# Kernel tuning notes

Measured on AMD Instinct MI355X. Metric: run time of the kernel, lower is better.

## Reference

```python
import jax, jax.numpy as jnp
import numpy as np

N, E, B, BLOCK = 100000, 1600000, 8, 12500
IN, HID, K, OUT = 128, 128, 4, 2
EPS = 1e-15


def setup_inputs() -> dict:
    key = jax.random.key(0)
    ks = jax.random.split(key, 14)
    x = jax.random.normal(ks[0], (N, IN), jnp.float32)
    # edges constrained within each graph's contiguous node block
    src = jax.random.randint(ks[1], (E,), 0, N)
    off = jax.random.randint(ks[2], (E,), 0, BLOCK)
    dst = (src // BLOCK) * BLOCK + off
    edge_index = jnp.stack([src, dst])
    batch = jnp.arange(N) // BLOCK
    s = 0.02
    params = dict(
        W_root1=jax.random.normal(ks[3], (IN, HID), jnp.float32) * s,
        W_rel1=jax.random.normal(ks[4], (IN, HID), jnp.float32) * s,
        b_rel1=jnp.zeros((HID,), jnp.float32),
        W_pool=jax.random.normal(ks[5], (HID, K), jnp.float32) * s,
        b_pool=jnp.zeros((K,), jnp.float32),
        W_rel3=jax.random.normal(ks[6], (HID, HID), jnp.float32) * s,
        b_rel3=jnp.zeros((HID,), jnp.float32),
        W_root3=jax.random.normal(ks[7], (HID, HID), jnp.float32) * s,
        W_lin1=jax.random.normal(ks[8], (HID, HID), jnp.float32) * s,
        b_lin1=jnp.zeros((HID,), jnp.float32),
        W_lin2=jax.random.normal(ks[9], (HID, OUT), jnp.float32) * s,
        b_lin2=jnp.zeros((OUT,), jnp.float32),
    )
    return dict(x=x, edge_index=edge_index, batch=batch, **params)


def _forward(x, edge_index, batch, W_root1, W_rel1, b_rel1, W_pool, b_pool,
             W_rel3, b_rel3, W_root3, W_lin1, b_lin1, W_lin2, b_lin2):
    src, dst = edge_index[0], edge_index[1]
    # GraphConv (aggr='add'): lin_rel(sum_j x_j) + lin_root(x)
    agg = jax.ops.segment_sum(x[src], dst, num_segments=N)  # [N, IN]
    h = jax.nn.relu(agg @ W_rel1 + b_rel1 + x @ W_root1)    # [N, HID]
    # cluster assignment
    s = jax.nn.softmax(h @ W_pool + b_pool, axis=-1)        # [N, K]
    # pooled node features: out[b] = S_b^T X_b  -> [B, K, HID]
    out = jax.ops.segment_sum(s[:, :, None] * h[:, None, :], batch, num_segments=B)
    # coarsened adjacency: out_adj[b] = S_b^T A_b S_b (A[dst, src] = 1 per edge)
    e_graph = batch[dst]
    contrib = s[dst][:, :, None] * s[src][:, None, :]       # [E, K, K]
    out_adj = jax.ops.segment_sum(contrib, e_graph, num_segments=B)  # [B, K, K]
    # mincut loss
    mincut_num = jnp.einsum('bkk->b', out_adj)
    deg = jax.ops.segment_sum(jnp.ones((E,), x.dtype), dst, num_segments=N)
    mincut_den = jax.ops.segment_sum(deg * jnp.sum(s * s, axis=-1), batch, num_segments=B)
    mc_loss = jnp.mean(-(mincut_num / mincut_den))
    # orthogonality loss
    ss = jax.ops.segment_sum(s[:, :, None] * s[:, None, :], batch, num_segments=B)  # [B,K,K]
    ss_norm = jnp.linalg.norm(ss, axis=(1, 2), keepdims=True)
    i_s = jnp.eye(K, dtype=x.dtype)
    o_loss = jnp.mean(jnp.linalg.norm(ss / ss_norm - i_s / jnp.sqrt(jnp.float32(K)), axis=(1, 2)))
    # fix and normalize coarsened adjacency
    out_adj = out_adj * (1.0 - i_s)  # zero diagonal
    d = jnp.sqrt(jnp.sum(out_adj, axis=-1)) + EPS  # [B, K]
    out_adj = out_adj / d[:, None, :] / d[:, :, None]
    # DenseGraphConv (aggr='add'): lin_rel(adj @ x) + lin_root(x)
    x2 = jnp.einsum('bkl,blc->bkc', out_adj, out) @ W_rel3 + b_rel3 + out @ W_root3
    x2 = jnp.mean(x2, axis=1)  # [B, HID]
    x2 = jax.nn.relu(x2 @ W_lin1 + b_lin1)
    logits = x2 @ W_lin2 + b_lin2
    return jax.nn.log_softmax(logits, axis=-1), mc_loss, o_loss, s, out_adj


def reference(x, edge_index, batch, W_root1, W_rel1, b_rel1, W_pool, b_pool,
              W_rel3, b_rel3, W_root3, W_lin1, b_lin1, W_lin2, b_lin2):
    return _forward(x, edge_index, batch, W_root1, W_rel1, b_rel1, W_pool, b_pool,
                    W_rel3, b_rel3, W_root3, W_lin1, b_lin1, W_lin2, b_lin2)
```

## Files before the change

kernel.cpp:

```cpp
#include <hip/hip_runtime.h>

#define NN     100000
#define EE     1600000
#define NB     8
#define BLK    12500
#define HID    128
#define KC     4
#define CHUNKS 196
#define NTILE  49
#define NBIN   392
#define GCAPS  5120

typedef __attribute__((ext_vector_type(8))) short bf16x8;
typedef __attribute__((ext_vector_type(4))) float f32x4;

__device__ __forceinline__ ushort f2bf(float f) {
  uint u = __float_as_uint(f);
  return (ushort)((u + 0x7FFFu + ((u >> 16) & 1u)) >> 16);
}
__device__ __forceinline__ float bf2f(ushort h) {
  return __uint_as_float(((uint)h) << 16);
}

#define GLL16(g, l) \
  __builtin_amdgcn_global_load_lds((const __attribute__((address_space(1))) void*)(g), \
                                   (__attribute__((address_space(3))) void*)(l), 16, 0, 0)

__global__ __launch_bounds__(256) void k_prep(const float4* __restrict__ x4,
                                              ushort* __restrict__ xb,
                                              const float* __restrict__ Wrel1,
                                              const float* __restrict__ Wroot1,
                                              ushort* __restrict__ Wt,
                                              uint* __restrict__ zbase) {
  const int bi = blockIdx.x;
  const int t = threadIdx.x;
  if (bi < 12500) {
    int i = bi * 256 + t;
    float4 v = x4[i];
    ushort4 r;
    r.x = f2bf(v.x); r.y = f2bf(v.y); r.z = f2bf(v.z); r.w = f2bf(v.w);
    *(ushort4*)(xb + (size_t)i * 4) = r;
  } else if (bi < 12628) {
    int col = bi - 12500, k = t;
    float v = (k < 128) ? Wrel1[k * 128 + col] : Wroot1[(k - 128) * 128 + col];
    Wt[col * 256 + k] = f2bf(v);
  } else {
    for (int i = t; i < 4912; i += 256) zbase[i] = 0u;
  }
}

__global__ __launch_bounds__(256) void k_bucket2(const int* __restrict__ ei,
                                                 int* __restrict__ sbcnt,
                                                 uint* __restrict__ gbuf) {
  __shared__ uint stage[8192];
  __shared__ int cnt[NBIN], start[NBIN + 1], rbase[NBIN];
  __shared__ int gtot[8], gb[8];
  const int t = threadIdx.x;
  for (int b = t; b < NBIN; b += 256) cnt[b] = 0;
  __syncthreads();
  const int e0 = blockIdx.x * 8192;
  uint pk[32]; int br[32];
#pragma unroll
  for (int i = 0; i < 32; ++i) {
    int e = e0 + i * 256 + t;
    bool val = (e < EE);
    int src = 0, dst = 0;
    if (val) {
      src = __builtin_nontemporal_load(ei + e);
      dst = __builtin_nontemporal_load(ei + EE + e);
    }
    int g = dst / BLK;
    int dl = dst - g * BLK;
    int sl = src - g * BLK;
    int bin = g * NTILE + (dl >> 8);
    pk[i] = ((uint)sl << 16) | (uint)dl;
    br[i] = val ? ((bin << 14) | atomicAdd(&cnt[bin], 1)) : -1;
  }
  __syncthreads();
  if (t < 8) {
    int s = 0;
    for (int k = 0; k < NTILE; ++k) s += cnt[t * NTILE + k];
    gtot[t] = s;
  }
  __syncthreads();
  if (t == 0) {
    int s = 0;
    for (int g = 0; g < 8; ++g) { gb[g] = s; s += gtot[g]; }
    start[NBIN] = s;
  }
  __syncthreads();
  if (t < 8) {
    int run = gb[t];
    for (int k = 0; k < NTILE; ++k) { start[t * NTILE + k] = run; run += cnt[t * NTILE + k]; }
  }
  __syncthreads();
  for (int b = t; b < NBIN; b += 256) rbase[b] = atomicAdd(&sbcnt[b], cnt[b]);
#pragma unroll
  for (int i = 0; i < 32; ++i) {
    if (br[i] >= 0) {
      int bin = br[i] >> 14, rank = br[i] & 16383;
      stage[start[bin] + rank] = pk[i];
    }
  }
  __syncthreads();
  for (int b = t; b < NBIN; b += 256) {
    const int n = cnt[b];
    const int s0 = start[b];
    uint* dst = gbuf + (size_t)b * GCAPS + rbase[b];
    for (int i = 0; i < n; ++i) dst[i] = stage[s0 + i];
  }
}

__global__ __launch_bounds__(256) void k_csr_tile(const uint* __restrict__ gbuf,
                                                  const int* __restrict__ sbcnt,
                                                  int* __restrict__ rowptr,
                                                  int* __restrict__ count,
                                                  int* __restrict__ csr) {
  const int g = blockIdx.x & 7;
  const int tile = blockIdx.x >> 3;
  const int bin = g * NTILE + tile;
  const int m = sbcnt[bin];
  const int n0t = tile * 256;
  const int nt = min(256, BLK - n0t);
  __shared__ uint ent[GCAPS];
  __shared__ ushort srt[GCAPS];
  __shared__ int cnt[256], scn[256], cur[256];
  __shared__ int red[256];
  const int t = threadIdx.x;
  {
    int partial = 0;
    for (int i = t; i < bin; i += 256) partial += sbcnt[i];
    red[t] = partial;
    __syncthreads();
    for (int off = 128; off > 0; off >>= 1) {
      if (t < off) red[t] += red[t + off];
      __syncthreads();
    }
  }
  const int base = red[0];
  cnt[t] = 0;
  __syncthreads();
  const uint* buf = gbuf + (size_t)bin * GCAPS;
  for (int i = t; i < m; i += 256) {
    uint pk = buf[i];
    ent[i] = pk;
    atomicAdd(&cnt[(int)(pk & 0xFFFFu) - n0t], 1);
  }
  __syncthreads();
  int v = cnt[t];
  scn[t] = v;
  __syncthreads();
  for (int s = 1; s < 256; s <<= 1) {
    int x = (t >= s) ? scn[t - s] : 0;
    __syncthreads();
    scn[t] += x;
    __syncthreads();
  }
  int excl = scn[t] - v;
  cur[t] = excl;
  if (t < nt) {
    rowptr[g * BLK + n0t + t] = base + excl;
    count[g * BLK + n0t + t] = v;
  }
  __syncthreads();
  for (int i = t; i < m; i += 256) {
    uint pk = ent[i];
    int p = atomicAdd(&cur[(int)(pk & 0xFFFFu) - n0t], 1);
    srt[p] = (ushort)(pk >> 16);
  }
  __syncthreads();
  const int nb = g * BLK;
  for (int i = t; i < m; i += 256)
    csr[base + i] = nb + (int)srt[i];
}

__global__ __launch_bounds__(256) void k_agg2(const ushort* __restrict__ xb,
                                              const int* __restrict__ count,
                                              const int* __restrict__ rowptr,
                                              const int* __restrict__ csr,
                                              const ushort* __restrict__ zrow,
                                              ushort* __restrict__ aggb) {
  const int xg = blockIdx.x & 7;
  const int j = blockIdx.x >> 3;
  const int half = threadIdx.x >> 5;
  const int lane = threadIdx.x & 31;
  const int ln = j * 8 + half;
  if (ln >= BLK) return;
  const int node = xg * BLK + ln;
  const int deg = count[node];
  const int* sl = csr + rowptr[node];
  int idx0 = (lane < deg) ? sl[lane] : 0;
  int idx1 = (32 + lane < deg) ? sl[32 + lane] : 0;
  const ushort* zr = zrow + lane * 4;

  float4 acc[8];
#pragma unroll
  for (int q = 0; q < 8; ++q) acc[q] = (float4){0.f, 0.f, 0.f, 0.f};

  const int nb8 = (deg + 7) >> 3;
  for (int b = 0; b < nb8; ++b) {
    const int e = b * 8;
    const ushort* ps[8];
#pragma unroll
    for (int q = 0; q < 8; ++q) {
      int ee = e + q;
      int si = (ee < 32) ? __shfl(idx0, ee, 32)
             : ((ee < 64) ? __shfl(idx1, ee - 32, 32)
                          : ((ee < deg) ? sl[ee] : 0));
      ps[q] = (ee < deg) ? (xb + (size_t)si * HID + lane * 4) : zr;
    }
    uint2 v[8];
#pragma unroll
    for (int q = 0; q < 8; ++q) v[q] = *(const uint2*)ps[q];
#pragma unroll
    for (int q = 0; q < 8; ++q) {
      acc[q].x += __uint_as_float(v[q].x << 16);
      acc[q].y += __uint_as_float(v[q].x & 0xFFFF0000u);
      acc[q].z += __uint_as_float(v[q].y << 16);
      acc[q].w += __uint_as_float(v[q].y & 0xFFFF0000u);
    }
  }

  float lo0 = 0.f, hi0 = 0.f, lo1 = 0.f, hi1 = 0.f;
#pragma unroll
  for (int q = 0; q < 8; ++q) { lo0 += acc[q].x; hi0 += acc[q].y; lo1 += acc[q].z; hi1 += acc[q].w; }
  ushort4 r;
  r.x = f2bf(lo0); r.y = f2bf(hi0); r.z = f2bf(lo1); r.w = f2bf(hi1);
  *(ushort4*)(aggb + (size_t)node * HID + lane * 4) = r;
}

__global__ __launch_bounds__(256) void k_gemm(
    const ushort* __restrict__ aggb, const ushort* __restrict__ xb,
    const ushort* __restrict__ Wt, const float* __restrict__ brel1,
    ushort* __restrict__ hbuf) {
  __shared__ ushort Aag_s[64][128];
  __shared__ ushort Ax_s[64][128];
  __shared__ ushort hLb[64][136];

  const int t = threadIdx.x;
  const int bi = blockIdx.x;
  const int bG = bi & 7;
  const int chunk = bi >> 3;
  const int node0 = bG * BLK + chunk * 64;
  int nrows = BLK - chunk * 64;
  if (nrows > 64) nrows = 64;

  const int w = t >> 6;
  const int l = t & 63;

  {
    const int sub = l >> 4;
    const int c16 = l & 15;
#pragma unroll
    for (int i = 0; i < 4; ++i) {
      const int j = w * 4 + i;
      const int row = j * 4 + sub;
      const int rs = (row < nrows) ? row : (nrows - 1);
      const int boff = (c16 * 16) ^ ((row & 7) << 4);
      const ushort* ga = aggb + (size_t)(node0 + rs) * HID + (boff >> 1);
      const ushort* gx = xb + (size_t)(node0 + rs) * HID + (boff >> 1);
      GLL16(ga, &Aag_s[j * 4][0]);
      GLL16(gx, &Ax_s[j * 4][0]);
    }
  }

  const int m16 = l & 15;
  const int gq = l >> 4;

  bf16x8 Breg[8][2];
#pragma unroll
  for (int kt = 0; kt < 8; ++kt)
#pragma unroll
    for (int fc = 0; fc < 2; ++fc)
      Breg[kt][fc] =
          *(const bf16x8*)(Wt + (size_t)(32 * w + 16 * fc + m16) * 256 + kt * 32 + 8 * gq);

  f32x4 acc[4][2];
#pragma unroll
  for (int fr = 0; fr < 4; ++fr)
#pragma unroll
    for (int fc = 0; fc < 2; ++fc) acc[fr][fc] = (f32x4){0.f, 0.f, 0.f, 0.f};

  asm volatile("s_waitcnt vmcnt(0)" ::: "memory");
  __syncthreads();

#pragma unroll
  for (int kt = 0; kt < 8; ++kt) {
    const int k4 = kt & 3;
    bf16x8 af[4];
#pragma unroll
    for (int fr = 0; fr < 4; ++fr) {
      const int r = 16 * fr + m16;
      const int ci = (k4 * 32 + gq * 8) ^ ((r & 7) << 3);
      af[fr] = (kt < 4) ? *(const bf16x8*)&Aag_s[r][ci]
                        : *(const bf16x8*)&Ax_s[r][ci];
    }
#pragma unroll
    for (int fr = 0; fr < 4; ++fr)
#pragma unroll
      for (int fc = 0; fc < 2; ++fc)
        acc[fr][fc] = __builtin_amdgcn_mfma_f32_16x16x32_bf16(af[fr], Breg[kt][fc],
                                                              acc[fr][fc], 0, 0, 0);
  }

  const float bc0 = brel1[32 * w + m16];
  const float bc1 = brel1[32 * w + 16 + m16];
#pragma unroll
  for (int fr = 0; fr < 4; ++fr)
#pragma unroll
    for (int fc = 0; fc < 2; ++fc)
#pragma unroll
      for (int r = 0; r < 4; ++r)
        hLb[16 * fr + 4 * gq + r][32 * w + 16 * fc + m16] =
            f2bf(fmaxf(acc[fr][fc][r] + (fc ? bc1 : bc0), 0.f));
  __syncthreads();

  {
    const int row = t >> 2;
    const int ch = (t & 3) * 32;
    if (row < nrows) {
      ushort* dst = hbuf + (size_t)(node0 + row) * HID + ch;
      const ushort* src = &hLb[row][ch];
#pragma unroll
      for (int q = 0; q < 4; ++q)
        *(bf16x8*)(dst + q * 8) = *(const bf16x8*)(src + q * 8);
    }
  }
}

__global__ __launch_bounds__(256) void k_epi(
    const ushort* __restrict__ hbuf, const float* __restrict__ Wpool,
    const float* __restrict__ bpool, const int* __restrict__ count,
    float* __restrict__ s_out, float* __restrict__ out_pool,
    float* __restrict__ ss_g, float* __restrict__ den_g) {
  __shared__ ushort hLb[64][136];
  __shared__ float outL[KC][HID];
  __shared__ float ssL[16];
  __shared__ float denL;

  const int t = threadIdx.x;
  const int bi = blockIdx.x;
  const int bG = bi & 7;
  const int chunk = bi >> 3;
  const int node0 = bG * BLK + chunk * 64;
  int nrows = BLK - chunk * 64;
  if (nrows > 64) nrows = 64;

  {
    const int row = t >> 2;
    const int ch = (t & 3) * 32;
    const int rs = (row < nrows) ? row : (nrows - 1);
    const ushort* src = hbuf + (size_t)(node0 + rs) * HID + ch;
    ushort* dst = &hLb[row][ch];
#pragma unroll
    for (int q = 0; q < 4; ++q)
      *(bf16x8*)(dst + q * 8) = *(const bf16x8*)(src + q * 8);
  }

  for (int i = t; i < KC * HID; i += 256) ((float*)outL)[i] = 0.f;
  if (t < 16) ssL[t] = 0.f;
  if (t == 0) denL = 0.f;
  __syncthreads();

  const int g4 = t >> 4;
  const int c0 = (t & 15) << 2;
  const int li = t & 15;

  float h[4][8];
#pragma unroll
  for (int r = 0; r < 4; ++r) {
    ushort4 v0 = *(const ushort4*)&hLb[g4 * 4 + r][c0];
    ushort4 v1 = *(const ushort4*)&hLb[g4 * 4 + r][c0 + 64];
    h[r][0] = bf2f(v0.x); h[r][1] = bf2f(v0.y); h[r][2] = bf2f(v0.z); h[r][3] = bf2f(v0.w);
    h[r][4] = bf2f(v1.x); h[r][5] = bf2f(v1.y); h[r][6] = bf2f(v1.z); h[r][7] = bf2f(v1.w);
  }

  float wp[8][4];
#pragma unroll
  for (int j = 0; j < 8; ++j) {
    int col = c0 + (j & 3) + (j >> 2) * 64;
    float4 v = *(const float4*)(Wpool + col * 4);
    wp[j][0] = v.x; wp[j][1] = v.y; wp[j][2] = v.z; wp[j][3] = v.w;
  }
  float pp[4][4];
#pragma unroll
  for (int r = 0; r < 4; ++r)
#pragma unroll
    for (int k = 0; k < 4; ++k) pp[r][k] = 0.f;
#pragma unroll
  for (int r = 0; r < 4; ++r)
#pragma unroll
    for (int j = 0; j < 8; ++j)
#pragma unroll
      for (int k = 0; k < 4; ++k) pp[r][k] = fmaf(h[r][j], wp[j][k], pp[r][k]);
#pragma unroll
  for (int m = 1; m <= 8; m <<= 1)
#pragma unroll
    for (int r = 0; r < 4; ++r)
#pragma unroll
      for (int k = 0; k < 4; ++k) pp[r][k] += __shfl_xor(pp[r][k], m);

  float4 bp4 = *(const float4*)bpool;
  float bp[4] = {bp4.x, bp4.y, bp4.z, bp4.w};
  float sv[4][4];
#pragma unroll
  for (int r = 0; r < 4; ++r) {
    float p[4];
#pragma unroll
    for (int k = 0; k < 4; ++k) p[k] = pp[r][k] + bp[k];
    float mx = fmaxf(fmaxf(p[0], p[1]), fmaxf(p[2], p[3]));
    float e0 = expf(p[0] - mx), e1 = expf(p[1] - mx), e2 = expf(p[2] - mx), e3 = expf(p[3] - mx);
    float inv = 1.f / (e0 + e1 + e2 + e3);
    float valid = (g4 * 4 + r < nrows) ? 1.f : 0.f;
    sv[r][0] = e0 * inv * valid; sv[r][1] = e1 * inv * valid;
    sv[r][2] = e2 * inv * valid; sv[r][3] = e3 * inv * valid;
  }

  {
    int rW = li >> 2, kW = li & 3;
    if (g4 * 4 + rW < nrows) {
      int node = node0 + g4 * 4 + rW;
      float val = 0.f;
#pragma unroll
      for (int rr = 0; rr < 4; ++rr)
#pragma unroll
        for (int kk = 0; kk < 4; ++kk)
          if (li == rr * 4 + kk) val = sv[rr][kk];
      s_out[node * 4 + kW] = val;
    }
  }

  {
    int k1 = li >> 2, k2 = li & 3;
    float a1[4], a2[4];
#pragma unroll
    for (int rr = 0; rr < 4; ++rr) {
      float v1 = 0.f, v2 = 0.f;
#pragma unroll
      for (int kk = 0; kk < 4; ++kk) {
        if (k1 == kk) v1 = sv[rr][kk];
        if (k2 == kk) v2 = sv[rr][kk];
      }
      a1[rr] = v1; a2[rr] = v2;
    }
    float ssv = a1[0] * a2[0] + a1[1] * a2[1] + a1[2] * a2[2] + a1[3] * a2[3];
    atomicAdd(&ssL[li], ssv);
  }

  if (li == 0) {
    float dent = 0.f;
#pragma unroll
    for (int rr = 0; rr < 4; ++rr) {
      int rowg = g4 * 4 + rr;
      if (rowg < nrows) {
        float dg = (float)count[node0 + rowg];
        dent += dg * (sv[rr][0] * sv[rr][0] + sv[rr][1] * sv[rr][1] +
                      sv[rr][2] * sv[rr][2] + sv[rr][3] * sv[rr][3]);
      }
    }
    atomicAdd(&denL, dent);
  }

  float po[4][8];
#pragma unroll
  for (int k = 0; k < 4; ++k)
#pragma unroll
    for (int c = 0; c < 8; ++c) po[k][c] = 0.f;
#pragma unroll
  for (int k = 0; k < 4; ++k)
#pragma unroll
    for (int rr = 0; rr < 4; ++rr)
#pragma unroll
      for (int c = 0; c < 8; ++c) po[k][c] = fmaf(sv[rr][k], h[rr][c], po[k][c]);
#pragma unroll
  for (int k = 0; k < 4; ++k)
#pragma unroll
    for (int c = 0; c < 8; ++c) {
      po[k][c] += __shfl_xor(po[k][c], 16);
      po[k][c] += __shfl_xor(po[k][c], 32);
    }
  if ((t & 63) < 16) {
#pragma unroll
    for (int k = 0; k < 4; ++k)
#pragma unroll
      for (int c = 0; c < 8; ++c)
        atomicAdd(&outL[k][c0 + (c & 3) + (c >> 2) * 64], po[k][c]);
  }

  __syncthreads();
  for (int i = t; i < KC * HID; i += 256)
    atomicAdd(&out_pool[bG * KC * HID + i], ((const float*)outL)[i]);
  if (t < 16) atomicAdd(&ss_g[bG * 16 + t], ssL[t]);
  if (t == 0) atomicAdd(&den_g[bG], denL);
}

__global__ __launch_bounds__(256) void k_adj2(const int* __restrict__ count,
                                              const int* __restrict__ rowptr,
                                              const int* __restrict__ csr,
                                              const float* __restrict__ s,
                                              const float* __restrict__ zf,
                                              float* __restrict__ adjraw) {
  __shared__ float accL[4][2][16];
  const int t = threadIdx.x;
  if (t < 128) ((float*)accL)[t] = 0.f;
  __syncthreads();
  const int node = blockIdx.x * 256 + t;
  const int g0 = (blockIdx.x * 256) / BLK;
  if (node < NN) {
    const int gi = node / BLK - g0;
    const int deg = count[node];
    const int* sl = csr + rowptr[node];
    float a[8][4];
#pragma unroll
    for (int q = 0; q < 8; ++q)
#pragma unroll
      for (int c = 0; c < 4; ++c) a[q][c] = 0.f;
    const int nb8 = (deg + 7) >> 3;
    for (int b = 0; b < nb8; ++b) {
      const float* p[8];
#pragma unroll
      for (int q = 0; q < 8; ++q) {
        int ee = b * 8 + q;
        int si = (ee < deg) ? sl[ee] : 0;
        p[q] = (ee < deg) ? (s + (size_t)si * 4) : zf;
      }
      float4 v[8];
#pragma unroll
      for (int q = 0; q < 8; ++q) v[q] = *(const float4*)p[q];
#pragma unroll
      for (int q = 0; q < 8; ++q) {
        a[q][0] += v[q].x; a[q][1] += v[q].y; a[q][2] += v[q].z; a[q][3] += v[q].w;
      }
    }
    float t0 = 0.f, t1 = 0.f, t2 = 0.f, t3 = 0.f;
#pragma unroll
    for (int q = 0; q < 8; ++q) { t0 += a[q][0]; t1 += a[q][1]; t2 += a[q][2]; t3 += a[q][3]; }
    float4 sn = *(const float4*)(s + (size_t)node * 4);
    float* base = accL[t >> 6][gi];
#pragma unroll
    for (int i = 0; i < 16; ++i) {
      int idx = (i + t) & 15;
      int hi = idx >> 2, lo = idx & 3;
      float a1 = (hi == 0) ? sn.x : (hi == 1) ? sn.y : (hi == 2) ? sn.z : sn.w;
      float b1 = (lo == 0) ? t0 : (lo == 1) ? t1 : (lo == 2) ? t2 : t3;
      atomicAdd(base + idx, a1 * b1);
    }
  }
  __syncthreads();
  if (t < 32) {
    int gi = t >> 4, i = t & 15, gg = g0 + gi;
    if (gg < NB) {
      float v = accL[0][gi][i] + accL[1][gi][i] + accL[2][gi][i] + accL[3][gi][i];
      atomicAdd(&adjraw[gg * 16 + i], v);
    }
  }
}

__global__ __launch_bounds__(1024) void k_tail(
    const float* __restrict__ out_pool, const float* __restrict__ adjraw,
    const float* __restrict__ den_g, const float* __restrict__ ss_g,
    const float* __restrict__ Wrel3, const float* __restrict__ brel3,
    const float* __restrict__ Wroot3, const float* __restrict__ Wlin1,
    const float* __restrict__ blin1, const float* __restrict__ Wlin2,
    const float* __restrict__ blin2, float* __restrict__ d_out,
    float* __restrict__ scratch) {
  const int g = threadIdx.x >> 7;
  const int tt = threadIdx.x & 127;
  __shared__ float adjL[NB][16], adjnL[NB][16], dL[NB][4];
  __shared__ float osL[NB][128], msL[NB][128], x2mL[NB][128], x3L[NB][128];
  if (tt < 16) adjL[g][tt] = adjraw[g * 16 + tt];
  __syncthreads();
  if (tt < 4) {
    float srow = 0.f;
#pragma unroll
    for (int l = 0; l < 4; ++l)
      if (l != tt) srow += adjL[g][tt * 4 + l];
    dL[g][tt] = sqrtf(srow) + 1e-15f;
  }
  __syncthreads();
  if (tt < 16) {
    int k1 = tt >> 2, k2 = tt & 3;
    float az = (k1 == k2) ? 0.f : adjL[g][tt];
    float an = az / (dL[g][k2] * dL[g][k1]);
    adjnL[g][tt] = an;
    d_out[400018 + g * 16 + tt] = an;
  }
  __syncthreads();
  float o0 = out_pool[g * 512 + 0 * 128 + tt];
  float o1 = out_pool[g * 512 + 1 * 128 + tt];
  float o2 = out_pool[g * 512 + 2 * 128 + tt];
  float o3 = out_pool[g * 512 + 3 * 128 + tt];
  float m0 = adjnL[g][0] * o0 + adjnL[g][1] * o1 + adjnL[g][2] * o2 + adjnL[g][3] * o3;
  float m1 = adjnL[g][4] * o0 + adjnL[g][5] * o1 + adjnL[g][6] * o2 + adjnL[g][7] * o3;
  float m2 = adjnL[g][8] * o0 + adjnL[g][9] * o1 + adjnL[g][10] * o2 + adjnL[g][11] * o3;
  float m3 = adjnL[g][12] * o0 + adjnL[g][13] * o1 + adjnL[g][14] * o2 + adjnL[g][15] * o3;
  osL[g][tt] = o0 + o1 + o2 + o3;
  msL[g][tt] = m0 + m1 + m2 + m3;
  __syncthreads();
  float accc = brel3[tt];
  for (int j = 0; j < 128; ++j)
    accc += 0.25f * (msL[g][j] * Wrel3[j * 128 + tt] + osL[g][j] * Wroot3[j * 128 + tt]);
  x2mL[g][tt] = accc;
  __syncthreads();
  float a2 = blin1[tt];
  for (int j = 0; j < 128; ++j) a2 += x2mL[g][j] * Wlin1[j * 128 + tt];
  x3L[g][tt] = fmaxf(a2, 0.f);
  __syncthreads();
  if (tt < 2) {
    float lg = blin2[tt];
    for (int j = 0; j < 128; ++j) lg += x3L[g][j] * Wlin2[j * 2 + tt];
    scratch[g * 2 + tt] = lg;
  }
  if (tt == 0) {
    float tr = adjL[g][0] + adjL[g][5] + adjL[g][10] + adjL[g][15];
    scratch[16 + g] = tr / den_g[g];
    float n2 = 0.f;
    for (int i = 0; i < 16; ++i) { float v = ss_g[g * 16 + i]; n2 += v * v; }
    float nn = sqrtf(n2);
    float od = 0.f;
    for (int i = 0; i < 16; ++i) {
      float v = ss_g[g * 16 + i] / nn - (((i >> 2) == (i & 3)) ? 0.5f : 0.f);
      od += v * v;
    }
    scratch[24 + g] = sqrtf(od);
  }
  __syncthreads();
  if (threadIdx.x == 0) {
    float mc = 0.f, oo = 0.f;
    for (int b = 0; b < NB; ++b) { mc += scratch[16 + b]; oo += scratch[24 + b]; }
    d_out[16] = -(mc / (float)NB);
    d_out[17] = oo / (float)NB;
    for (int b = 0; b < NB; ++b) {
      float l0 = scratch[2 * b], l1 = scratch[2 * b + 1];
      float m = fmaxf(l0, l1);
      float lse = m + logf(expf(l0 - m) + expf(l1 - m));
      d_out[2 * b] = l0 - lse;
      d_out[2 * b + 1] = l1 - lse;
    }
  }
}

extern "C" void kernel_launch(void* const* d_in, const int* in_sizes, int n_in,
                              void* d_out, int out_size, void* d_ws, size_t ws_size,
                              hipStream_t stream) {
  (void)in_sizes; (void)n_in; (void)out_size; (void)ws_size;
  const float* x      = (const float*)d_in[0];
  const int*   ei     = (const int*)d_in[1];
  const float* Wroot1 = (const float*)d_in[3];
  const float* Wrel1  = (const float*)d_in[4];
  const float* brel1  = (const float*)d_in[5];
  const float* Wpool  = (const float*)d_in[6];
  const float* bpool  = (const float*)d_in[7];
  const float* Wrel3  = (const float*)d_in[8];
  const float* brel3  = (const float*)d_in[9];
  const float* Wroot3 = (const float*)d_in[10];
  const float* Wlin1  = (const float*)d_in[11];
  const float* blin1  = (const float*)d_in[12];
  const float* Wlin2  = (const float*)d_in[13];
  const float* blin2  = (const float*)d_in[14];
  float* out = (float*)d_out;

  char* ws = (char*)d_ws;
  float*  out_pool = (float*)(ws + 0);
  float*  ss_g     = (float*)(ws + 16384);
  float*  adjraw   = (float*)(ws + 16896);
  float*  den_g    = (float*)(ws + 17408);
  float*  scratch  = (float*)(ws + 17440);
  int*    sbcnt    = (int*)(ws + 17568);
  ushort* zrow     = (ushort*)(ws + 19136);
  float*  zf       = (float*)(ws + 19392);
  int*    count    = (int*)(ws + 21248);
  int*    rowptr   = (int*)(ws + 421248);
  ushort* Wt       = (ushort*)(ws + 821264);
  int*    csr      = (int*)(ws + 886800);
  ushort* xb       = (ushort*)(ws + 7286800);
  ushort* aggb     = (ushort*)(ws + 32886800);
  uint*   gbuf     = (uint*)(ws + 58486800);
  ushort* hbuf     = (ushort*)(ws + 66514960);

  k_prep<<<12629, 256, 0, stream>>>((const float4*)x, xb, Wrel1, Wroot1, Wt,
                                    (uint*)ws);
  k_bucket2<<<196, 256, 0, stream>>>(ei, sbcnt, gbuf);
  k_csr_tile<<<NBIN, 256, 0, stream>>>(gbuf, sbcnt, rowptr, count, csr);
  k_agg2<<<8 * ((BLK + 7) / 8), 256, 0, stream>>>(xb, count, rowptr, csr, zrow, aggb);
  k_gemm<<<NB * CHUNKS, 256, 0, stream>>>(aggb, xb, Wt, brel1, hbuf);
  k_epi<<<NB * CHUNKS, 256, 0, stream>>>(hbuf, Wpool, bpool, count, out + 18,
                                         out_pool, ss_g, den_g);
  k_adj2<<<(NN + 255) / 256, 256, 0, stream>>>(count, rowptr, csr, out + 18, zf, adjraw);
  k_tail<<<1, 1024, 0, stream>>>(out_pool, adjraw, den_g, ss_g, Wrel3, brel3, Wroot3,
                                 Wlin1, blin1, Wlin2, blin2, out, scratch);
}
```

Before: 202.6 us.

## Merge prep with bucketing, move softmax into GEMM, fuse pooling with adjacency

```diff
diff --git a/kernel.cpp b/kernel.cpp
--- a/kernel.cpp
+++ b/kernel.cpp
@@ -31,34 +31,32 @@
                                               const float* __restrict__ Wrel1,
                                               const float* __restrict__ Wroot1,
                                               ushort* __restrict__ Wt,
-                                              uint* __restrict__ zbase) {
-  const int bi = blockIdx.x;
-  const int t = threadIdx.x;
-  if (bi < 12500) {
-    int i = bi * 256 + t;
-    float4 v = x4[i];
-    ushort4 r;
-    r.x = f2bf(v.x); r.y = f2bf(v.y); r.z = f2bf(v.z); r.w = f2bf(v.w);
-    *(ushort4*)(xb + (size_t)i * 4) = r;
-  } else if (bi < 12628) {
-    int col = bi - 12500, k = t;
-    float v = (k < 128) ? Wrel1[k * 128 + col] : Wroot1[(k - 128) * 128 + col];
-    Wt[col * 256 + k] = f2bf(v);
-  } else {
-    for (int i = t; i < 4912; i += 256) zbase[i] = 0u;
-  }
-}
-
-__global__ __launch_bounds__(256) void k_bucket2(const int* __restrict__ ei,
-                                                 int* __restrict__ sbcnt,
-                                                 uint* __restrict__ gbuf) {
+                                              const int* __restrict__ ei,
+                                              int* __restrict__ sbcnt,
+                                              uint* __restrict__ gbuf) {
   __shared__ uint stage[8192];
   __shared__ int cnt[NBIN], start[NBIN + 1], rbase[NBIN];
   __shared__ int gtot[8], gb[8];
+  const int bi = blockIdx.x;
   const int t = threadIdx.x;
+  if (bi >= 196) {
+    const int pb = bi - 196;
+    if (pb < 12500) {
+      int i = pb * 256 + t;
+      float4 v = x4[i];
+      ushort4 r;
+      r.x = f2bf(v.x); r.y = f2bf(v.y); r.z = f2bf(v.z); r.w = f2bf(v.w);
+      *(ushort4*)(xb + (size_t)i * 4) = r;
+    } else {
+      int col = pb - 12500, k = t;
+      float v = (k < 128) ? Wrel1[k * 128 + col] : Wroot1[(k - 128) * 128 + col];
+      Wt[col * 256 + k] = f2bf(v);
+    }
+    return;
+  }
   for (int b = t; b < NBIN; b += 256) cnt[b] = 0;
   __syncthreads();
-  const int e0 = blockIdx.x * 8192;
+  const int e0 = bi * 8192;
   uint pk[32]; int br[32];
 #pragma unroll
   for (int i = 0; i < 32; ++i) {
@@ -232,7 +230,8 @@
 __global__ __launch_bounds__(256) void k_gemm(
     const ushort* __restrict__ aggb, const ushort* __restrict__ xb,
     const ushort* __restrict__ Wt, const float* __restrict__ brel1,
-    ushort* __restrict__ hbuf) {
+    const float* __restrict__ Wpool, const float* __restrict__ bpool,
+    ushort* __restrict__ hbuf, float* __restrict__ s_out) {
   __shared__ ushort Aag_s[64][128];
   __shared__ ushort Ax_s[64][128];
   __shared__ ushort hLb[64][136];
@@ -326,20 +325,133 @@
         *(bf16x8*)(dst + q * 8) = *(const bf16x8*)(src + q * 8);
     }
   }
-}
-
-__global__ __launch_bounds__(256) void k_epi(
-    const ushort* __restrict__ hbuf, const float* __restrict__ Wpool,
-    const float* __restrict__ bpool, const int* __restrict__ count,
-    float* __restrict__ s_out, float* __restrict__ out_pool,
-    float* __restrict__ ss_g, float* __restrict__ den_g) {
+
+  const int g4 = t >> 4;
+  const int c0 = (t & 15) << 2;
+  const int li = t & 15;
+
+  float h[4][8];
+#pragma unroll
+  for (int r = 0; r < 4; ++r) {
+    ushort4 v0 = *(const ushort4*)&hLb[g4 * 4 + r][c0];
+    ushort4 v1 = *(const ushort4*)&hLb[g4 * 4 + r][c0 + 64];
+    h[r][0] = bf2f(v0.x); h[r][1] = bf2f(v0.y); h[r][2] = bf2f(v0.z); h[r][3] = bf2f(v0.w);
+    h[r][4] = bf2f(v1.x); h[r][5] = bf2f(v1.y); h[r][6] = bf2f(v1.z); h[r][7] = bf2f(v1.w);
+  }
+  float wp[8][4];
+#pragma unroll
+  for (int j = 0; j < 8; ++j) {
+    int col = c0 + (j & 3) + (j >> 2) * 64;
+    float4 v = *(const float4*)(Wpool + col * 4);
+    wp[j][0] = v.x; wp[j][1] = v.y; wp[j][2] = v.z; wp[j][3] = v.w;
+  }
+  float pp[4][4];
+#pragma unroll
+  for (int r = 0; r < 4; ++r)
+#pragma unroll
+    for (int k = 0; k < 4; ++k) pp[r][k] = 0.f;
+#pragma unroll
+  for (int r = 0; r < 4; ++r)
+#pragma unroll
+    for (int j = 0; j < 8; ++j)
+#pragma unroll
+      for (int k = 0; k < 4; ++k) pp[r][k] = fmaf(h[r][j], wp[j][k], pp[r][k]);
+#pragma unroll
+  for (int m = 1; m <= 8; m <<= 1)
+#pragma unroll
+    for (int r = 0; r < 4; ++r)
+#pragma unroll
+      for (int k = 0; k < 4; ++k) pp[r][k] += __shfl_xor(pp[r][k], m);
+
+  float4 bp4 = *(const float4*)bpool;
+  float bp[4] = {bp4.x, bp4.y, bp4.z, bp4.w};
+#pragma unroll
+  for (int r = 0; r < 4; ++r) {
+    float p[4];
+#pragma unroll
+    for (int k = 0; k < 4; ++k) p[k] = pp[r][k] + bp[k];
+    float mx = fmaxf(fmaxf(p[0], p[1]), fmaxf(p[2], p[3]));
+    float e0 = expf(p[0] - mx), e1 = expf(p[1] - mx), e2 = expf(p[2] - mx), e3 = expf(p[3] - mx);
+    float inv = 1.f / (e0 + e1 + e2 + e3);
+    int rW = li >> 2, kW = li & 3;
+    if (r == rW && g4 * 4 + rW < nrows) {
+      float val = (kW == 0) ? e0 * inv : (kW == 1) ? e1 * inv : (kW == 2) ? e2 * inv : e3 * inv;
+      s_out[(node0 + g4 * 4 + rW) * 4 + kW] = val;
+    }
+  }
+}
+
+__global__ __launch_bounds__(256) void k_epiadj(
+    const ushort* __restrict__ hbuf, const float* __restrict__ s_in,
+    const int* __restrict__ count, const int* __restrict__ rowptr,
+    const int* __restrict__ csr, const float* __restrict__ zf,
+    float* __restrict__ out_pool, float* __restrict__ ss_g,
+    float* __restrict__ den_g, float* __restrict__ adjraw) {
   __shared__ ushort hLb[64][136];
   __shared__ float outL[KC][HID];
   __shared__ float ssL[16];
   __shared__ float denL;
-
+  __shared__ float accL[4][2][16];
   const int t = threadIdx.x;
   const int bi = blockIdx.x;
+
+  if (bi >= NB * CHUNKS) {
+    const int abi = bi - NB * CHUNKS;
+    if (t < 128) ((float*)accL)[t] = 0.f;
+    __syncthreads();
+    const int node = abi * 256 + t;
+    const int g0 = (abi * 256) / BLK;
+    if (node < NN) {
+      const int gi = node / BLK - g0;
+      const int deg = count[node];
+      const int* sl = csr + rowptr[node];
+      float a[8][4];
+#pragma unroll
+      for (int q = 0; q < 8; ++q)
+#pragma unroll
+        for (int c = 0; c < 4; ++c) a[q][c] = 0.f;
+      const int nb8 = (deg + 7) >> 3;
+      for (int b = 0; b < nb8; ++b) {
+        const float* p[8];
+#pragma unroll
+        for (int q = 0; q < 8; ++q) {
+          int ee = b * 8 + q;
+          int si = (ee < deg) ? sl[ee] : 0;
+          p[q] = (ee < deg) ? (s_in + (size_t)si * 4) : zf;
+        }
+        float4 v[8];
+#pragma unroll
+        for (int q = 0; q < 8; ++q) v[q] = *(const float4*)p[q];
+#pragma unroll
+        for (int q = 0; q < 8; ++q) {
+          a[q][0] += v[q].x; a[q][1] += v[q].y; a[q][2] += v[q].z; a[q][3] += v[q].w;
+        }
+      }
+      float t0 = 0.f, t1 = 0.f, t2 = 0.f, t3 = 0.f;
+#pragma unroll
+      for (int q = 0; q < 8; ++q) { t0 += a[q][0]; t1 += a[q][1]; t2 += a[q][2]; t3 += a[q][3]; }
+      float4 sn = *(const float4*)(s_in + (size_t)node * 4);
+      float* base = accL[t >> 6][gi];
+#pragma unroll
+      for (int i = 0; i < 16; ++i) {
+        int idx = (i + t) & 15;
+        int hi = idx >> 2, lo = idx & 3;
+        float a1 = (hi == 0) ? sn.x : (hi == 1) ? sn.y : (hi == 2) ? sn.z : sn.w;
+        float b1 = (lo == 0) ? t0 : (lo == 1) ? t1 : (lo == 2) ? t2 : t3;
+        atomicAdd(base + idx, a1 * b1);
+      }
+    }
+    __syncthreads();
+    if (t < 32) {
+      int gi = t >> 4, i = t & 15, gg = g0 + gi;
+      if (gg < NB) {
+        float v = accL[0][gi][i] + accL[1][gi][i] + accL[2][gi][i] + accL[3][gi][i];
+        atomicAdd(&adjraw[gg * 16 + i], v);
+      }
+    }
+    return;
+  }
+
   const int bG = bi & 7;
   const int chunk = bi >> 3;
   const int node0 = bG * BLK + chunk * 64;
@@ -375,59 +487,13 @@
     h[r][4] = bf2f(v1.x); h[r][5] = bf2f(v1.y); h[r][6] = bf2f(v1.z); h[r][7] = bf2f(v1.w);
   }
 
-  float wp[8][4];
-#pragma unroll
-  for (int j = 0; j < 8; ++j) {
-    int col = c0 + (j & 3) + (j >> 2) * 64;
-    float4 v = *(const float4*)(Wpool + col * 4);
-    wp[j][0] = v.x; wp[j][1] = v.y; wp[j][2] = v.z; wp[j][3] = v.w;
-  }
-  float pp[4][4];
-#pragma unroll
-  for (int r = 0; r < 4; ++r)
-#pragma unroll
-    for (int k = 0; k < 4; ++k) pp[r][k] = 0.f;
-#pragma unroll
-  for (int r = 0; r < 4; ++r)
-#pragma unroll
-    for (int j = 0; j < 8; ++j)
-#pragma unroll
-      for (int k = 0; k < 4; ++k) pp[r][k] = fmaf(h[r][j], wp[j][k], pp[r][k]);
-#pragma unroll
-  for (int m = 1; m <= 8; m <<= 1)
-#pragma unroll
-    for (int r = 0; r < 4; ++r)
-#pragma unroll
-      for (int k = 0; k < 4; ++k) pp[r][k] += __shfl_xor(pp[r][k], m);
-
-  float4 bp4 = *(const float4*)bpool;
-  float bp[4] = {bp4.x, bp4.y, bp4.z, bp4.w};
   float sv[4][4];
 #pragma unroll
   for (int r = 0; r < 4; ++r) {
-    float p[4];
-#pragma unroll
-    for (int k = 0; k < 4; ++k) p[k] = pp[r][k] + bp[k];
-    float mx = fmaxf(fmaxf(p[0], p[1]), fmaxf(p[2], p[3]));
-    float e0 = expf(p[0] - mx), e1 = expf(p[1] - mx), e2 = expf(p[2] - mx), e3 = expf(p[3] - mx);
-    float inv = 1.f / (e0 + e1 + e2 + e3);
-    float valid = (g4 * 4 + r < nrows) ? 1.f : 0.f;
-    sv[r][0] = e0 * inv * valid; sv[r][1] = e1 * inv * valid;
-    sv[r][2] = e2 * inv * valid; sv[r][3] = e3 * inv * valid;
-  }
-
-  {
-    int rW = li >> 2, kW = li & 3;
-    if (g4 * 4 + rW < nrows) {
-      int node = node0 + g4 * 4 + rW;
-      float val = 0.f;
-#pragma unroll
-      for (int rr = 0; rr < 4; ++rr)
-#pragma unroll
-        for (int kk = 0; kk < 4; ++kk)
-          if (li == rr * 4 + kk) val = sv[rr][kk];
-      s_out[node * 4 + kW] = val;
-    }
+    int rowg = g4 * 4 + r;
+    float4 sval = (float4){0.f, 0.f, 0.f, 0.f};
+    if (rowg < nrows) sval = *(const float4*)(s_in + (size_t)(node0 + rowg) * 4);
+    sv[r][0] = sval.x; sv[r][1] = sval.y; sv[r][2] = sval.z; sv[r][3] = sval.w;
   }
 
   {
@@ -492,68 +558,6 @@
     atomicAdd(&out_pool[bG * KC * HID + i], ((const float*)outL)[i]);
   if (t < 16) atomicAdd(&ss_g[bG * 16 + t], ssL[t]);
   if (t == 0) atomicAdd(&den_g[bG], denL);
-}
-
-__global__ __launch_bounds__(256) void k_adj2(const int* __restrict__ count,
-                                              const int* __restrict__ rowptr,
-                                              const int* __restrict__ csr,
-                                              const float* __restrict__ s,
-                                              const float* __restrict__ zf,
-                                              float* __restrict__ adjraw) {
-  __shared__ float accL[4][2][16];
-  const int t = threadIdx.x;
-  if (t < 128) ((float*)accL)[t] = 0.f;
-  __syncthreads();
-  const int node = blockIdx.x * 256 + t;
-  const int g0 = (blockIdx.x * 256) / BLK;
-  if (node < NN) {
-    const int gi = node / BLK - g0;
-    const int deg = count[node];
-    const int* sl = csr + rowptr[node];
-    float a[8][4];
-#pragma unroll
-    for (int q = 0; q < 8; ++q)
-#pragma unroll
-      for (int c = 0; c < 4; ++c) a[q][c] = 0.f;
-    const int nb8 = (deg + 7) >> 3;
-    for (int b = 0; b < nb8; ++b) {
-      const float* p[8];
-#pragma unroll
-      for (int q = 0; q < 8; ++q) {
-        int ee = b * 8 + q;
-        int si = (ee < deg) ? sl[ee] : 0;
-        p[q] = (ee < deg) ? (s + (size_t)si * 4) : zf;
-      }
-      float4 v[8];
-#pragma unroll
-      for (int q = 0; q < 8; ++q) v[q] = *(const float4*)p[q];
-#pragma unroll
-      for (int q = 0; q < 8; ++q) {
-        a[q][0] += v[q].x; a[q][1] += v[q].y; a[q][2] += v[q].z; a[q][3] += v[q].w;
-      }
-    }
-    float t0 = 0.f, t1 = 0.f, t2 = 0.f, t3 = 0.f;
-#pragma unroll
-    for (int q = 0; q < 8; ++q) { t0 += a[q][0]; t1 += a[q][1]; t2 += a[q][2]; t3 += a[q][3]; }
-    float4 sn = *(const float4*)(s + (size_t)node * 4);
-    float* base = accL[t >> 6][gi];
-#pragma unroll
-    for (int i = 0; i < 16; ++i) {
-      int idx = (i + t) & 15;
-      int hi = idx >> 2, lo = idx & 3;
-      float a1 = (hi == 0) ? sn.x : (hi == 1) ? sn.y : (hi == 2) ? sn.z : sn.w;
-      float b1 = (lo == 0) ? t0 : (lo == 1) ? t1 : (lo == 2) ? t2 : t3;
-      atomicAdd(base + idx, a1 * b1);
-    }
-  }
-  __syncthreads();
-  if (t < 32) {
-    int gi = t >> 4, i = t & 15, gg = g0 + gi;
-    if (gg < NB) {
-      float v = accL[0][gi][i] + accL[1][gi][i] + accL[2][gi][i] + accL[3][gi][i];
-      atomicAdd(&adjraw[gg * 16 + i], v);
-    }
-  }
 }
 
 __global__ __launch_bounds__(1024) void k_tail(
@@ -678,15 +682,15 @@
   uint*   gbuf     = (uint*)(ws + 58486800);
   ushort* hbuf     = (ushort*)(ws + 66514960);
 
-  k_prep<<<12629, 256, 0, stream>>>((const float4*)x, xb, Wrel1, Wroot1, Wt,
-                                    (uint*)ws);
-  k_bucket2<<<196, 256, 0, stream>>>(ei, sbcnt, gbuf);
+  hipMemsetAsync(ws, 0, 19648, stream);
+  k_prep<<<196 + 12500 + 128, 256, 0, stream>>>((const float4*)x, xb, Wrel1, Wroot1,
+                                                Wt, ei, sbcnt, gbuf);
   k_csr_tile<<<NBIN, 256, 0, stream>>>(gbuf, sbcnt, rowptr, count, csr);
   k_agg2<<<8 * ((BLK + 7) / 8), 256, 0, stream>>>(xb, count, rowptr, csr, zrow, aggb);
-  k_gemm<<<NB * CHUNKS, 256, 0, stream>>>(aggb, xb, Wt, brel1, hbuf);
-  k_epi<<<NB * CHUNKS, 256, 0, stream>>>(hbuf, Wpool, bpool, count, out + 18,
-                                         out_pool, ss_g, den_g);
-  k_adj2<<<(NN + 255) / 256, 256, 0, stream>>>(count, rowptr, csr, out + 18, zf, adjraw);
+  k_gemm<<<NB * CHUNKS, 256, 0, stream>>>(aggb, xb, Wt, brel1, Wpool, bpool, hbuf,
+                                          out + 18);
+  k_epiadj<<<NB * CHUNKS + (NN + 255) / 256, 256, 0, stream>>>(
+      hbuf, out + 18, count, rowptr, csr, zf, out_pool, ss_g, den_g, adjraw);
   k_tail<<<1, 1024, 0, stream>>>(out_pool, adjraw, den_g, ss_g, Wrel3, brel3, Wroot3,
                                  Wlin1, blin1, Wlin2, blin2, out, scratch);
 }
```

Result: faster. 180.6 us (median of 2 runs) (-10.8%).
